# Optimization experiments

Measured on AMD Instinct MI355X. Metric: run time of the kernel, lower is better.

The kernel has to match this reference:

```python
import jax, jax.numpy as jnp
import numpy as np

N_NODES = 100000
IN_FEATS = 512
H_FEATS = 128
N_HOPS = 3
N_NIE = N_HOPS + 1  # 4 per-hop branches
N_EDGES = 1600000


def _layernorm(z, g, b, eps=1e-5):
    mu = jnp.mean(z, axis=-1, keepdims=True)
    var = jnp.var(z, axis=-1, keepdims=True)
    return (z - mu) * jax.lax.rsqrt(var + eps) * g + b


def _mlp(z, W, b, g, be):
    # Dropout(p=0) -> Linear -> LayerNorm -> ReLU (eval mode)
    return jax.nn.relu(_layernorm(z @ W + b, g, be))


def setup_inputs() -> dict:
    key = jax.random.key(0)
    ks = jax.random.split(key, 16)
    ei = jax.random.randint(ks[0], (2, N_EDGES), 0, N_NODES, dtype=jnp.int64)
    feats = jax.random.normal(ks[1], (N_NODES, IN_FEATS), dtype=jnp.float32)
    s_in = 1.0 / np.sqrt(IN_FEATS)
    s_h = 1.0 / np.sqrt(H_FEATS)
    s_c = 1.0 / np.sqrt(N_NIE * H_FEATS)
    return {
        "edge_index": ei,
        "features": feats,
        # unified input transform (transform_first=True): in_feats -> h_feats
        "W_uni": jax.random.normal(ks[2], (IN_FEATS, H_FEATS), jnp.float32) * s_in,
        "b_uni": jnp.zeros((H_FEATS,), jnp.float32),
        "g_uni": jnp.ones((H_FEATS,), jnp.float32),
        "be_uni": jnp.zeros((H_FEATS,), jnp.float32),
        # per-hop independent embeddings: h_feats -> h_feats, one per hop (stacked)
        "W_ind": jax.random.normal(ks[3], (N_NIE, H_FEATS, H_FEATS), jnp.float32) * s_h,
        "b_ind": jnp.zeros((N_NIE, H_FEATS), jnp.float32),
        "g_ind": jnp.ones((N_NIE, H_FEATS), jnp.float32),
        "be_ind": jnp.zeros((N_NIE, H_FEATS), jnp.float32),
        # relation network (RN='concat'): ndim_fc -> h_feats
        "W_rel": jax.random.normal(ks[4], (N_NIE * H_FEATS, H_FEATS), jnp.float32) * s_c,
        "b_rel": jnp.zeros((H_FEATS,), jnp.float32),
        "g_rel": jnp.ones((H_FEATS,), jnp.float32),
        "be_rel": jnp.zeros((H_FEATS,), jnp.float32),
    }


def reference(edge_index, features, W_uni, b_uni, g_uni, be_uni,
              W_ind, b_ind, g_ind, be_ind, W_rel, b_rel, g_rel, be_rel):
    N = features.shape[0]
    # F.normalize(features, dim=1)  (row_normalized=True)
    x = features / jnp.maximum(
        jnp.linalg.norm(features, axis=1, keepdims=True), 1e-12)

    # preprocess_adj: add self loops, then symmetric normalization D^-1/2 A D^-1/2
    loops = jnp.arange(N, dtype=edge_index.dtype)
    row = jnp.concatenate([edge_index[0], loops])
    col = jnp.concatenate([edge_index[1], loops])
    deg = jax.ops.segment_sum(jnp.ones_like(row, dtype=x.dtype), row,
                              num_segments=N)
    dinv = jnp.where(deg > 0, deg ** -0.5, 0.0)
    w = dinv[row] * dinv[col]  # [E+N] edge weights

    def spmm(z):
        # out[row] += w * z[col]   (gather + scatter-add, memory-bound)
        return jax.ops.segment_sum(w[:, None] * z[col], row, num_segments=N)

    # transform_first: unified embedding before multi-hop aggregation
    h = _mlp(x, W_uni, b_uni, g_uni, be_uni)  # [N, H]

    # inceptive aggregation: hop-0 is h itself, hop-i = A^i h; per-hop MLPs
    z = h
    ns = [_mlp(z, W_ind[0], b_ind[0], g_ind[0], be_ind[0])]
    for i in range(1, N_NIE):
        z = spmm(z)
        ns.append(_mlp(z, W_ind[i], b_ind[i], g_ind[i], be_ind[i]))

    cat = jnp.concatenate(ns, axis=1)  # [N, 4*H]
    out = _mlp(cat, W_rel, b_rel, g_rel, be_rel)  # [N, H]
    return out
```

## Files before the change

kernel.cpp:

```cpp
#include <hip/hip_runtime.h>
#include <hip/hip_bf16.h>

#define NN 100000
#define FE 512
#define HF 128
#define NE 1600000
#define NNIE 4
#define BCAP 64
#define NSLC 8

typedef __attribute__((ext_vector_type(8))) __bf16 bf16x8;
typedef __attribute__((ext_vector_type(4))) float f32x4;
typedef __attribute__((ext_vector_type(8))) unsigned short ushort8;

__device__ __forceinline__ unsigned short f2bf(float f) {
    unsigned u = __float_as_uint(f);
    unsigned r = (u + 0x7fffu + ((u >> 16) & 1u)) >> 16;
    return (unsigned short)r;
}
__device__ __forceinline__ float b2f(unsigned short u) {
    return __uint_as_float(((unsigned)u) << 16);
}

__global__ __launch_bounds__(256) void k_zero(int* __restrict__ cursor, int n) {
    int i = blockIdx.x * 256 + threadIdx.x;
    if (i < n) cursor[i] = 0;
}

__global__ __launch_bounds__(256) void k_fill(const int* __restrict__ rows,
                                              const int* __restrict__ cols,
                                              int* __restrict__ cursor,
                                              int* __restrict__ es, int e) {
    const int grp = blockIdx.x & (NSLC - 1);
    const int sub = blockIdx.x >> 3;
    const int r_lo = grp * (NN / NSLC);
    const int r_hi = r_lo + (NN / NSLC);
    const int tpg = (gridDim.x >> 3) * 256;

    for (int i0 = (sub * 256 + (int)threadIdx.x) * 4; i0 + 3 < e;
         i0 += tpg * 4) {
        const int4 rr = *(const int4*)(rows + i0);
        const int r4[4] = {rr.x, rr.y, rr.z, rr.w};
#pragma unroll
        for (int u = 0; u < 4; u++) {
            const int r = r4[u];
            if (r >= r_lo && r < r_hi) {
                const int c = cols[i0 + u];
                const int pos = atomicAdd(&cursor[r], 1);
                if (pos < BCAP) es[(r << 6) + pos] = c;
            }
        }
    }
}

__global__ __launch_bounds__(256) void k_dinv(const int* __restrict__ cursor,
                                              float* __restrict__ dinv, int n) {
    int i = blockIdx.x * 256 + threadIdx.x;
    if (i < n) dinv[i] = rsqrtf((float)(cursor[i] + 1));
}

__global__ __launch_bounds__(256) void k_wt_all(
    const float* __restrict__ Wu, const float* __restrict__ Wr,
    const float* __restrict__ Wi, unsigned short* __restrict__ Tu,
    unsigned short* __restrict__ Tr, unsigned short* __restrict__ Ti) {
    int i = blockIdx.x * 256 + threadIdx.x;
    if (i < 65536) {
        int k = i >> 7, n = i & 127;
        Tu[n * 512 + k] = f2bf(Wu[i]);
    } else if (i < 131072) {
        int j = i - 65536;
        int k = j >> 7, n = j & 127;
        Tr[n * 512 + k] = f2bf(Wr[j]);
    } else if (i < 196608) {
        int j = i - 131072;
        int hh = j >> 14, r = j & 16383;
        int k = r >> 7, n = r & 127;
        Ti[hh * 16384 + n * 128 + k] = f2bf(Wi[j]);
    }
}

__global__ __launch_bounds__(256) void k_spmm(
    const unsigned short* __restrict__ z, unsigned short* __restrict__ y,
    const int* __restrict__ cnt, const int* __restrict__ es,
    const float* __restrict__ dinv, int n) {
    const int node = blockIdx.x * 4 + (threadIdx.x >> 6);
    if (node >= n) return;
    const int lane = threadIdx.x & 63;
    const int g = lane >> 4;
    const int l = lane & 15;

    const float dr = dinv[node];
    int deg = cnt[node];
    if (deg > BCAP) deg = BCAP;
    const int* __restrict__ base = es + ((size_t)node << 6);

    float acc[8];
#pragma unroll
    for (int j = 0; j < 8; j++) acc[j] = 0.0f;

    for (int k0 = 4 * g; k0 < deg; k0 += 16) {
        const int4 cc = *(const int4*)(base + k0);
        const int ce[4] = {cc.x, cc.y, cc.z, cc.w};
#pragma unroll
        for (int e = 0; e < 4; e++) {
            const bool vld = (k0 + e) < deg;
            const int c = vld ? ce[e] : node;
            const float wc = vld ? dinv[c] : 0.0f;
            const ushort8 t = *(const ushort8*)(z + (size_t)c * HF + 8 * l);
#pragma unroll
            for (int j = 0; j < 8; j++) acc[j] = fmaf(wc, b2f(t[j]), acc[j]);
        }
    }
    if (g == 0) {
        const ushort8 v = *(const ushort8*)(z + (size_t)node * HF + 8 * l);
#pragma unroll
        for (int j = 0; j < 8; j++) acc[j] = fmaf(dr, b2f(v[j]), acc[j]);
    }
#pragma unroll
    for (int j = 0; j < 8; j++) {
        acc[j] += __shfl_xor(acc[j], 16);
        acc[j] += __shfl_xor(acc[j], 32);
    }
    if (g == 0) {
        ushort8 o;
#pragma unroll
        for (int j = 0; j < 8; j++) o[j] = f2bf(acc[j] * dr);
        *(ushort8*)(y + (size_t)node * HF + 8 * l) = o;
    }
}

__global__ __launch_bounds__(256) void gemm_uni(
    const float* __restrict__ A, const unsigned short* __restrict__ Wt,
    const float* __restrict__ bias, const float* __restrict__ g,
    const float* __restrict__ be, unsigned short* __restrict__ out, int M) {
    constexpr int K = FE;
    constexpr int LDT = 72;
    __shared__ unsigned short Ast[64][LDT];
    __shared__ unsigned short Bst[128][LDT];
    __shared__ float rn_s[64];

    const int tid = threadIdx.x;
    const int row0 = blockIdx.x * 64;
    const int w = tid >> 6;
    const int lane = tid & 63;
    const int m = lane & 15;
    const int q = lane >> 4;
    const int lrow = tid >> 2;
    const int lq = tid & 3;

    f32x4 acc[8];
#pragma unroll
    for (int t = 0; t < 8; t++) acc[t] = (f32x4){0.f, 0.f, 0.f, 0.f};

    float sumsq = 0.0f;
    const bool arow_ok = (row0 + lrow) < M;

    for (int k0 = 0; k0 < K; k0 += 64) {
        __syncthreads();
#pragma unroll
        for (int oo = 0; oo < 2; oo++) {
            const int o = lq + 4 * oo;
            f32x4 a0 = (f32x4){0.f, 0.f, 0.f, 0.f}, a1 = a0;
            if (arow_ok) {
                const float* Ap =
                    A + (size_t)(row0 + lrow) * K + k0 + 8 * o;
                a0 = *(const f32x4*)Ap;
                a1 = *(const f32x4*)(Ap + 4);
            }
#pragma unroll
            for (int j = 0; j < 4; j++) sumsq += a0[j] * a0[j] + a1[j] * a1[j];
            ushort8 pk;
#pragma unroll
            for (int j = 0; j < 4; j++) {
                pk[j] = f2bf(a0[j]);
                pk[j + 4] = f2bf(a1[j]);
            }
            *(ushort8*)&Ast[lrow][8 * o] = pk;
        }
        const int bn = tid >> 1;
#pragma unroll
        for (int kk = 0; kk < 4; kk++) {
            const int o = (tid & 1) + 2 * kk;
            *(ushort8*)&Bst[bn][8 * o] =
                *(const ushort8*)(Wt + (size_t)bn * K + k0 + 8 * o);
        }
        __syncthreads();
#pragma unroll
        for (int jj = 0; jj < 2; jj++) {
            bf16x8 af = *(const bf16x8*)&Ast[16 * w + m][8 * q + 32 * jj];
#pragma unroll
            for (int t = 0; t < 8; t++) {
                bf16x8 bfv = *(const bf16x8*)&Bst[16 * t + m][8 * q + 32 * jj];
                acc[t] = __builtin_amdgcn_mfma_f32_16x16x32_bf16(af, bfv,
                                                                 acc[t], 0, 0,
                                                                 0);
            }
        }
    }

    sumsq += __shfl_xor(sumsq, 1);
    sumsq += __shfl_xor(sumsq, 2);
    if (lq == 0) rn_s[lrow] = 1.0f / fmaxf(sqrtf(sumsq), 1e-12f);
    __syncthreads();

    float bb[8], gg[8], ee[8];
#pragma unroll
    for (int t = 0; t < 8; t++) {
        bb[t] = bias[16 * t + m];
        gg[t] = g[16 * t + m];
        ee[t] = be[16 * t + m];
    }
#pragma unroll
    for (int r = 0; r < 4; r++) {
        const int lrow2 = 16 * w + 4 * q + r;
        const float rn = rn_s[lrow2];
        float s1 = 0.f, s2 = 0.f;
#pragma unroll
        for (int t = 0; t < 8; t++) {
            float y = fmaf(acc[t][r], rn, bb[t]);
            s1 += y;
            s2 = fmaf(y, y, s2);
        }
#pragma unroll
        for (int mask = 1; mask <= 8; mask <<= 1) {
            s1 += __shfl_xor(s1, mask);
            s2 += __shfl_xor(s2, mask);
        }
        const float mean = s1 * (1.0f / 128.0f);
        const float var = fmaxf(s2 * (1.0f / 128.0f) - mean * mean, 0.0f);
        const float rstd = rsqrtf(var + 1e-5f);
        const int grow = row0 + lrow2;
        if (grow < M) {
#pragma unroll
            for (int t = 0; t < 8; t++) {
                float y = fmaf(acc[t][r], rn, bb[t]);
                float o = fmaxf(fmaf((y - mean) * rstd, gg[t], ee[t]), 0.0f);
                out[(size_t)grow * HF + 16 * t + m] = f2bf(o);
            }
        }
    }
}

__global__ __launch_bounds__(256) void k_tail(
    const unsigned short* __restrict__ z0, const unsigned short* __restrict__ z1,
    const unsigned short* __restrict__ z2, const unsigned short* __restrict__ z3,
    const unsigned short* __restrict__ Wt_ind,
    const float* __restrict__ b_ind, const float* __restrict__ g_ind,
    const float* __restrict__ be_ind,
    const unsigned short* __restrict__ Wt_rel,
    const float* __restrict__ b_rel, const float* __restrict__ g_rel,
    const float* __restrict__ be_rel, float* __restrict__ out, int M) {
    constexpr int LDW = 136;
    __shared__ unsigned short Wst[128][LDW];
    __shared__ unsigned short nsT[64][LDW];

    const int tid = threadIdx.x;
    const int row0 = blockIdx.x * 64;
    const int w = tid >> 6;
    const int lane = tid & 63;
    const int m = lane & 15;
    const int q = lane >> 4;
    const int bn = tid >> 1;

    const unsigned short* zs[4] = {z0, z1, z2, z3};

    f32x4 acc2[8];
#pragma unroll
    for (int t = 0; t < 8; t++) acc2[t] = (f32x4){0.f, 0.f, 0.f, 0.f};

    int arow = row0 + 16 * w + m;
    if (arow >= M) arow = M - 1;

#pragma unroll
    for (int hop = 0; hop < NNIE; hop++) {
        __syncthreads();
        const unsigned short* Wi = Wt_ind + hop * HF * HF;
#pragma unroll
        for (int k = 0; k < 8; k++) {
            const int o = (tid & 1) + 2 * k;
            *(ushort8*)&Wst[bn][8 * o] =
                *(const ushort8*)(Wi + (size_t)bn * HF + 8 * o);
        }
        __syncthreads();
        f32x4 acc[8];
#pragma unroll
        for (int t = 0; t < 8; t++) acc[t] = (f32x4){0.f, 0.f, 0.f, 0.f};
        const unsigned short* zp = zs[hop] + (size_t)arow * HF;
#pragma unroll
        for (int jj = 0; jj < 4; jj++) {
            bf16x8 af = *(const bf16x8*)(zp + 8 * q + 32 * jj);
#pragma unroll
            for (int t = 0; t < 8; t++) {
                bf16x8 bfv = *(const bf16x8*)&Wst[16 * t + m][8 * q + 32 * jj];
                acc[t] = __builtin_amdgcn_mfma_f32_16x16x32_bf16(af, bfv,
                                                                 acc[t], 0, 0,
                                                                 0);
            }
        }
        float bb[8], gg[8], ee[8];
#pragma unroll
        for (int t = 0; t < 8; t++) {
            bb[t] = b_ind[hop * HF + 16 * t + m];
            gg[t] = g_ind[hop * HF + 16 * t + m];
            ee[t] = be_ind[hop * HF + 16 * t + m];
        }
#pragma unroll
        for (int r = 0; r < 4; r++) {
            const int lrow2 = 16 * w + 4 * q + r;
            float s1 = 0.f, s2 = 0.f;
#pragma unroll
            for (int t = 0; t < 8; t++) {
                float y = acc[t][r] + bb[t];
                s1 += y;
                s2 = fmaf(y, y, s2);
            }
#pragma unroll
            for (int mask = 1; mask <= 8; mask <<= 1) {
                s1 += __shfl_xor(s1, mask);
                s2 += __shfl_xor(s2, mask);
            }
            const float mean = s1 * (1.0f / 128.0f);
            const float var = fmaxf(s2 * (1.0f / 128.0f) - mean * mean, 0.0f);
            const float rstd = rsqrtf(var + 1e-5f);
#pragma unroll
            for (int t = 0; t < 8; t++) {
                float y = acc[t][r] + bb[t];
                float o = fmaxf(fmaf((y - mean) * rstd, gg[t], ee[t]), 0.0f);
                nsT[lrow2][16 * t + m] = f2bf(o);
            }
        }
        __syncthreads();
#pragma unroll
        for (int k = 0; k < 8; k++) {
            const int o = (tid & 1) + 2 * k;
            *(ushort8*)&Wst[bn][8 * o] =
                *(const ushort8*)(Wt_rel + (size_t)bn * (NNIE * HF) +
                                  HF * hop + 8 * o);
        }
        __syncthreads();
#pragma unroll
        for (int jj = 0; jj < 4; jj++) {
            bf16x8 af = *(const bf16x8*)&nsT[16 * w + m][8 * q + 32 * jj];
#pragma unroll
            for (int t = 0; t < 8; t++) {
                bf16x8 bfv = *(const bf16x8*)&Wst[16 * t + m][8 * q + 32 * jj];
                acc2[t] = __builtin_amdgcn_mfma_f32_16x16x32_bf16(af, bfv,
                                                                  acc2[t], 0,
                                                                  0, 0);
            }
        }
    }

    float bb[8], gg[8], ee[8];
#pragma unroll
    for (int t = 0; t < 8; t++) {
        bb[t] = b_rel[16 * t + m];
        gg[t] = g_rel[16 * t + m];
        ee[t] = be_rel[16 * t + m];
    }
#pragma unroll
    for (int r = 0; r < 4; r++) {
        const int lrow2 = 16 * w + 4 * q + r;
        float s1 = 0.f, s2 = 0.f;
#pragma unroll
        for (int t = 0; t < 8; t++) {
            float y = acc2[t][r] + bb[t];
            s1 += y;
            s2 = fmaf(y, y, s2);
        }
#pragma unroll
        for (int mask = 1; mask <= 8; mask <<= 1) {
            s1 += __shfl_xor(s1, mask);
            s2 += __shfl_xor(s2, mask);
        }
        const float mean = s1 * (1.0f / 128.0f);
        const float var = fmaxf(s2 * (1.0f / 128.0f) - mean * mean, 0.0f);
        const float rstd = rsqrtf(var + 1e-5f);
        const int grow = row0 + lrow2;
        if (grow < M) {
#pragma unroll
            for (int t = 0; t < 8; t++) {
                float y = acc2[t][r] + bb[t];
                float o = fmaxf(fmaf((y - mean) * rstd, gg[t], ee[t]), 0.0f);
                out[(size_t)grow * HF + 16 * t + m] = o;
            }
        }
    }
}

extern "C" void kernel_launch(void* const* d_in, const int* in_sizes, int n_in,
                              void* d_out, int out_size, void* d_ws,
                              size_t ws_size, hipStream_t stream) {
    const int* ei = (const int*)d_in[0];
    const float* feats = (const float*)d_in[1];
    const float* W_uni = (const float*)d_in[2];
    const float* b_uni = (const float*)d_in[3];
    const float* g_uni = (const float*)d_in[4];
    const float* be_uni = (const float*)d_in[5];
    const float* W_ind = (const float*)d_in[6];
    const float* b_ind = (const float*)d_in[7];
    const float* g_ind = (const float*)d_in[8];
    const float* be_ind = (const float*)d_in[9];
    const float* W_rel = (const float*)d_in[10];
    const float* b_rel = (const float*)d_in[11];
    const float* g_rel = (const float*)d_in[12];
    const float* be_rel = (const float*)d_in[13];
    float* out = (float*)d_out;

    char* p = (char*)d_ws;
    auto alloc = [&](size_t bytes) {
        void* r = (void*)p;
        p += (bytes + 255) & ~(size_t)255;
        return r;
    };
    int* cursor = (int*)alloc(NN * 4);
    int* es = (int*)alloc((size_t)NN * BCAP * 4);
    float* dinv = (float*)alloc(NN * 4);
    unsigned short* Wt_uni = (unsigned short*)alloc(128 * FE * 2);
    unsigned short* Wt_rel = (unsigned short*)alloc(128 * (NNIE * HF) * 2);
    unsigned short* Wt_ind = (unsigned short*)alloc(NNIE * HF * HF * 2);
    unsigned short* h = (unsigned short*)alloc((size_t)NN * HF * 2);
    unsigned short* za = (unsigned short*)alloc((size_t)NN * HF * 2);
    unsigned short* zb = (unsigned short*)alloc((size_t)NN * HF * 2);
    unsigned short* zc = (unsigned short*)alloc((size_t)NN * HF * 2);

    const int gN = (NN + 255) / 256;
    const int gGemm = (NN + 63) / 64;
    const int gSpmm = (NN + 3) / 4;
    const int gFill = 8 * 512;
    const int* erow = ei;
    const int* ecol = ei + NE;

    k_zero<<<gN, 256, 0, stream>>>(cursor, NN);
    k_fill<<<gFill, 256, 0, stream>>>(erow, ecol, cursor, es, NE);
    k_dinv<<<gN, 256, 0, stream>>>(cursor, dinv, NN);

    k_wt_all<<<(196608 + 255) / 256, 256, 0, stream>>>(W_uni, W_rel, W_ind,
                                                       Wt_uni, Wt_rel, Wt_ind);

    gemm_uni<<<gGemm, 256, 0, stream>>>(feats, Wt_uni, b_uni, g_uni, be_uni, h,
                                        NN);
    k_spmm<<<gSpmm, 256, 0, stream>>>(h, za, cursor, es, dinv, NN);
    k_spmm<<<gSpmm, 256, 0, stream>>>(za, zb, cursor, es, dinv, NN);
    k_spmm<<<gSpmm, 256, 0, stream>>>(zb, zc, cursor, es, dinv, NN);

    k_tail<<<gGemm, 256, 0, stream>>>(h, za, zb, zc, Wt_ind, b_ind, g_ind,
                                      be_ind, Wt_rel, b_rel, g_rel, be_rel,
                                      out, NN);
}
```

Baseline: 701.1 us.

## Fuse small setup kernels and load GEMM A operand directly to registers

Merges cursor zeroing into the weight-transpose kernel and moves the dinv computation into gemm_uni, which removes two launches. gemm_uni now has each lane load its fp32 feature row straight from global memory into MFMA registers, converting to bf16 and accumulating the row norm there, so the A tile no longer goes through LDS. The spmm self-row load is also hoisted ahead of the neighbor loop to overlap its latency. The direct A loads are less coalesced per wave than the old cooperative tile load, which risks lower memory efficiency on the 200MB feature read.

```diff
diff --git a/kernel.cpp b/kernel.cpp
--- a/kernel.cpp
+++ b/kernel.cpp
@@ -22,48 +22,13 @@
     return __uint_as_float(((unsigned)u) << 16);
 }
 
-__global__ __launch_bounds__(256) void k_zero(int* __restrict__ cursor, int n) {
-    int i = blockIdx.x * 256 + threadIdx.x;
-    if (i < n) cursor[i] = 0;
-}
-
-__global__ __launch_bounds__(256) void k_fill(const int* __restrict__ rows,
-                                              const int* __restrict__ cols,
-                                              int* __restrict__ cursor,
-                                              int* __restrict__ es, int e) {
-    const int grp = blockIdx.x & (NSLC - 1);
-    const int sub = blockIdx.x >> 3;
-    const int r_lo = grp * (NN / NSLC);
-    const int r_hi = r_lo + (NN / NSLC);
-    const int tpg = (gridDim.x >> 3) * 256;
-
-    for (int i0 = (sub * 256 + (int)threadIdx.x) * 4; i0 + 3 < e;
-         i0 += tpg * 4) {
-        const int4 rr = *(const int4*)(rows + i0);
-        const int r4[4] = {rr.x, rr.y, rr.z, rr.w};
-#pragma unroll
-        for (int u = 0; u < 4; u++) {
-            const int r = r4[u];
-            if (r >= r_lo && r < r_hi) {
-                const int c = cols[i0 + u];
-                const int pos = atomicAdd(&cursor[r], 1);
-                if (pos < BCAP) es[(r << 6) + pos] = c;
-            }
-        }
-    }
-}
-
-__global__ __launch_bounds__(256) void k_dinv(const int* __restrict__ cursor,
-                                              float* __restrict__ dinv, int n) {
-    int i = blockIdx.x * 256 + threadIdx.x;
-    if (i < n) dinv[i] = rsqrtf((float)(cursor[i] + 1));
-}
-
-__global__ __launch_bounds__(256) void k_wt_all(
+__global__ __launch_bounds__(256) void k_wt_zero(
     const float* __restrict__ Wu, const float* __restrict__ Wr,
     const float* __restrict__ Wi, unsigned short* __restrict__ Tu,
-    unsigned short* __restrict__ Tr, unsigned short* __restrict__ Ti) {
+    unsigned short* __restrict__ Tr, unsigned short* __restrict__ Ti,
+    int* __restrict__ cursor) {
     int i = blockIdx.x * 256 + threadIdx.x;
+    if (i < NN) cursor[i] = 0;
     if (i < 65536) {
         int k = i >> 7, n = i & 127;
         Tu[n * 512 + k] = f2bf(Wu[i]);
@@ -79,6 +44,32 @@
     }
 }
 
+__global__ __launch_bounds__(256) void k_fill(const int* __restrict__ rows,
+                                              const int* __restrict__ cols,
+                                              int* __restrict__ cursor,
+                                              int* __restrict__ es, int e) {
+    const int grp = blockIdx.x & (NSLC - 1);
+    const int sub = blockIdx.x >> 3;
+    const int r_lo = grp * (NN / NSLC);
+    const int r_hi = r_lo + (NN / NSLC);
+    const int tpg = (gridDim.x >> 3) * 256;
+
+    for (int i0 = (sub * 256 + (int)threadIdx.x) * 4; i0 + 3 < e;
+         i0 += tpg * 4) {
+        const int4 rr = *(const int4*)(rows + i0);
+        const int r4[4] = {rr.x, rr.y, rr.z, rr.w};
+#pragma unroll
+        for (int u = 0; u < 4; u++) {
+            const int r = r4[u];
+            if (r >= r_lo && r < r_hi) {
+                const int c = cols[i0 + u];
+                const int pos = atomicAdd(&cursor[r], 1);
+                if (pos < BCAP) es[(r << 6) + pos] = c;
+            }
+        }
+    }
+}
+
 __global__ __launch_bounds__(256) void k_spmm(
     const unsigned short* __restrict__ z, unsigned short* __restrict__ y,
     const int* __restrict__ cnt, const int* __restrict__ es,
@@ -94,13 +85,15 @@
     if (deg > BCAP) deg = BCAP;
     const int* __restrict__ base = es + ((size_t)node << 6);
 
+    const ushort8 vself = *(const ushort8*)(z + (size_t)node * HF + 8 * l);
+
     float acc[8];
 #pragma unroll
     for (int j = 0; j < 8; j++) acc[j] = 0.0f;
 
     for (int k0 = 4 * g; k0 < deg; k0 += 16) {
-        const int4 cc = *(const int4*)(base + k0);
-        const int ce[4] = {cc.x, cc.y, cc.z, cc.w};
+        const int4 cc4 = *(const int4*)(base + k0);
+        const int ce[4] = {cc4.x, cc4.y, cc4.z, cc4.w};
 #pragma unroll
         for (int e = 0; e < 4; e++) {
             const bool vld = (k0 + e) < deg;
@@ -112,9 +105,8 @@
         }
     }
     if (g == 0) {
-        const ushort8 v = *(const ushort8*)(z + (size_t)node * HF + 8 * l);
-#pragma unroll
-        for (int j = 0; j < 8; j++) acc[j] = fmaf(dr, b2f(v[j]), acc[j]);
+#pragma unroll
+        for (int j = 0; j < 8; j++) acc[j] = fmaf(dr, b2f(vself[j]), acc[j]);
     }
 #pragma unroll
     for (int j = 0; j < 8; j++) {
@@ -132,51 +124,38 @@
 __global__ __launch_bounds__(256) void gemm_uni(
     const float* __restrict__ A, const unsigned short* __restrict__ Wt,
     const float* __restrict__ bias, const float* __restrict__ g,
-    const float* __restrict__ be, unsigned short* __restrict__ out, int M) {
+    const float* __restrict__ be, unsigned short* __restrict__ out,
+    const int* __restrict__ cnt, float* __restrict__ dinv, int M) {
     constexpr int K = FE;
     constexpr int LDT = 72;
-    __shared__ unsigned short Ast[64][LDT];
     __shared__ unsigned short Bst[128][LDT];
     __shared__ float rn_s[64];
 
     const int tid = threadIdx.x;
     const int row0 = blockIdx.x * 64;
+
+    if (tid < 64) {
+        const int r = row0 + tid;
+        if (r < M) dinv[r] = rsqrtf((float)(cnt[r] + 1));
+    }
+
     const int w = tid >> 6;
     const int lane = tid & 63;
     const int m = lane & 15;
     const int q = lane >> 4;
-    const int lrow = tid >> 2;
-    const int lq = tid & 3;
+
+    int arow = row0 + 16 * w + m;
+    if (arow >= M) arow = M - 1;
+    const float* __restrict__ Ap = A + (size_t)arow * K;
 
     f32x4 acc[8];
 #pragma unroll
     for (int t = 0; t < 8; t++) acc[t] = (f32x4){0.f, 0.f, 0.f, 0.f};
 
     float sumsq = 0.0f;
-    const bool arow_ok = (row0 + lrow) < M;
 
     for (int k0 = 0; k0 < K; k0 += 64) {
         __syncthreads();
-#pragma unroll
-        for (int oo = 0; oo < 2; oo++) {
-            const int o = lq + 4 * oo;
-            f32x4 a0 = (f32x4){0.f, 0.f, 0.f, 0.f}, a1 = a0;
-            if (arow_ok) {
-                const float* Ap =
-                    A + (size_t)(row0 + lrow) * K + k0 + 8 * o;
-                a0 = *(const f32x4*)Ap;
-                a1 = *(const f32x4*)(Ap + 4);
-            }
-#pragma unroll
-            for (int j = 0; j < 4; j++) sumsq += a0[j] * a0[j] + a1[j] * a1[j];
-            ushort8 pk;
-#pragma unroll
-            for (int j = 0; j < 4; j++) {
-                pk[j] = f2bf(a0[j]);
-                pk[j + 4] = f2bf(a1[j]);
-            }
-            *(ushort8*)&Ast[lrow][8 * o] = pk;
-        }
         const int bn = tid >> 1;
 #pragma unroll
         for (int kk = 0; kk < 4; kk++) {
@@ -187,20 +166,29 @@
         __syncthreads();
 #pragma unroll
         for (int jj = 0; jj < 2; jj++) {
-            bf16x8 af = *(const bf16x8*)&Ast[16 * w + m][8 * q + 32 * jj];
+            const float* ap = Ap + k0 + 8 * q + 32 * jj;
+            const f32x4 a0 = *(const f32x4*)ap;
+            const f32x4 a1 = *(const f32x4*)(ap + 4);
+            union { ushort8 u; bf16x8 b; } cvt;
+#pragma unroll
+            for (int j = 0; j < 4; j++) {
+                sumsq += a0[j] * a0[j] + a1[j] * a1[j];
+                cvt.u[j] = f2bf(a0[j]);
+                cvt.u[j + 4] = f2bf(a1[j]);
+            }
 #pragma unroll
             for (int t = 0; t < 8; t++) {
                 bf16x8 bfv = *(const bf16x8*)&Bst[16 * t + m][8 * q + 32 * jj];
-                acc[t] = __builtin_amdgcn_mfma_f32_16x16x32_bf16(af, bfv,
+                acc[t] = __builtin_amdgcn_mfma_f32_16x16x32_bf16(cvt.b, bfv,
                                                                  acc[t], 0, 0,
                                                                  0);
             }
         }
     }
 
-    sumsq += __shfl_xor(sumsq, 1);
-    sumsq += __shfl_xor(sumsq, 2);
-    if (lq == 0) rn_s[lrow] = 1.0f / fmaxf(sqrtf(sumsq), 1e-12f);
+    sumsq += __shfl_xor(sumsq, 16);
+    sumsq += __shfl_xor(sumsq, 32);
+    if (q == 0) rn_s[16 * w + m] = 1.0f / fmaxf(sqrtf(sumsq), 1e-12f);
     __syncthreads();
 
     float bb[8], gg[8], ee[8];
@@ -424,26 +412,20 @@
     unsigned short* zb = (unsigned short*)alloc((size_t)NN * HF * 2);
     unsigned short* zc = (unsigned short*)alloc((size_t)NN * HF * 2);
 
-    const int gN = (NN + 255) / 256;
     const int gGemm = (NN + 63) / 64;
     const int gSpmm = (NN + 3) / 4;
     const int gFill = 8 * 512;
     const int* erow = ei;
     const int* ecol = ei + NE;
 
-    k_zero<<<gN, 256, 0, stream>>>(cursor, NN);
+    k_wt_zero<<<(196608 + 255) / 256, 256, 0, stream>>>(
+        W_uni, W_rel, W_ind, Wt_uni, Wt_rel, Wt_ind, cursor);
     k_fill<<<gFill, 256, 0, stream>>>(erow, ecol, cursor, es, NE);
-    k_dinv<<<gN, 256, 0, stream>>>(cursor, dinv, NN);
-
-    k_wt_all<<<(196608 + 255) / 256, 256, 0, stream>>>(W_uni, W_rel, W_ind,
-                                                       Wt_uni, Wt_rel, Wt_ind);
-
     gemm_uni<<<gGemm, 256, 0, stream>>>(feats, Wt_uni, b_uni, g_uni, be_uni, h,
-                                        NN);
+                                        cursor, dinv, NN);
     k_spmm<<<gSpmm, 256, 0, stream>>>(h, za, cursor, es, dinv, NN);
     k_spmm<<<gSpmm, 256, 0, stream>>>(za, zb, cursor, es, dinv, NN);
     k_spmm<<<gSpmm, 256, 0, stream>>>(zb, zc, cursor, es, dinv, NN);
-
     k_tail<<<gGemm, 256, 0, stream>>>(h, za, zb, zc, Wt_ind, b_ind, g_ind,
                                       be_ind, Wt_rel, b_rel, g_rel, be_rel,
                                       out, NN);
```

After: 704.8 us. No clear change (+0.5%).
